# Kernel optimization log

Hardware: AMD Instinct MI355X
Metric: run time of the kernel (lower is better)

## Reference

```python
import jax, jax.numpy as jnp
import numpy as np
import math

B, S, D, H, M = 2, 2048, 1024, 16, 64
HD = D // H  # head_dim = 64


def setup_inputs() -> dict:
    key = jax.random.key(0)
    ks = jax.random.split(key, 16)
    inp = {
        "query": jax.random.normal(ks[0], (B, S, D), jnp.float32),
        "key": jax.random.normal(ks[1], (B, S, D), jnp.float32),
        "value": jax.random.normal(ks[2], (B, S, D), jnp.float32),
        "mask": jax.random.randint(ks[3], (B, 1, 1, S), 0, 2, jnp.int32),
        "Wq": jax.random.normal(ks[4], (D, D), jnp.float32) * 0.02,
        "bq": jnp.zeros((D,), jnp.float32),
        "Wk": jax.random.normal(ks[5], (D, D), jnp.float32) * 0.02,
        "bk": jnp.zeros((D,), jnp.float32),
        "Wv": jax.random.normal(ks[6], (D, D), jnp.float32) * 0.02,
        "bv": jnp.zeros((D,), jnp.float32),
        "Wo": jax.random.normal(ks[7], (D, D), jnp.float32) * 0.02,
        "bo": jnp.zeros((D,), jnp.float32),
        "m_k": jax.random.normal(ks[8], (1, M, D), jnp.float32) * (1.0 / HD),
        "m_v": jax.random.normal(ks[9], (1, M, D), jnp.float32) * (1.0 / M),
    }
    return inp


def reference(query, key, value, mask, Wq, bq, Wk, bk, Wv, bv, Wo, bo, m_k, m_v):
    b, nq, d = query.shape
    nk = key.shape[1]
    h, hd, m = H, HD, M
    scale = math.sqrt(hd)

    Q = query @ Wq.T + bq                      # [b, nq, d]
    K = key @ Wk.T + bk                        # [b, nk, d]
    V = value @ Wv.T + bv                      # [b, nk, d]

    mk = scale * jnp.broadcast_to(m_k, (b, m, d))           # sqrt(head_dim)*m_k
    mv = math.sqrt(m) * jnp.broadcast_to(m_v, (b, m, d))    # sqrt(m)*m_v

    K = jnp.concatenate([K, mk], axis=1)       # [b, nk+m, d]
    V = jnp.concatenate([V, mv], axis=1)

    Qh = Q.reshape(b, nq, h, hd).transpose(0, 2, 1, 3)           # [b,h,nq,hd]
    Kh = K.reshape(b, nk + m, h, hd).transpose(0, 2, 1, 3)       # [b,h,nk+m,hd]
    Vh = V.reshape(b, nk + m, h, hd).transpose(0, 2, 1, 3)

    energy = jnp.einsum('bhqd,bhkd->bhqk', Qh, Kh) / scale       # [b,h,nq,nk+m]
    # mask only the first nk key columns; memory slots are never masked
    masked = jnp.where(mask == 0, jnp.float32(-1e20), energy[..., :nk])
    energy = jnp.concatenate([masked, energy[..., nk:]], axis=-1)

    attention = jax.nn.softmax(energy, axis=-1)
    x = jnp.einsum('bhqk,bhkd->bhqd', attention, Vh)             # [b,h,nq,hd]
    x = x.transpose(0, 2, 1, 3).reshape(b, nq, d)
    return x @ Wo.T + bo
```

## Files before the change

kernel.cpp:

```cpp
#include <hip/hip_runtime.h>
#include <hip/hip_bf16.h>
#include <stdint.h>

#define B_  2
#define S_  2048
#define D_  1024
#define H_  16
#define HD_ 64
#define M_  64
#define SKM (S_ + M_)
#define LOG2E 1.44269504088896340736f

typedef __attribute__((ext_vector_type(8))) short s16x8;
typedef __attribute__((ext_vector_type(4))) float f32x4;
typedef __attribute__((ext_vector_type(16))) float f32x16;

#define GLOAD16(gp, lp) __builtin_amdgcn_global_load_lds( \
    (const __attribute__((address_space(1))) void*)(gp),  \
    (__attribute__((address_space(3))) void*)(lp), 16, 0, 0)

#define WAITVM(N) do { asm volatile("s_waitcnt vmcnt(" #N ")" ::: "memory"); \
                       __builtin_amdgcn_sched_barrier(0); } while (0)
#define BARRIER() do { asm volatile("" ::: "memory"); \
                       __builtin_amdgcn_s_barrier(); \
                       asm volatile("" ::: "memory"); } while (0)

__device__ __forceinline__ unsigned short f2bf(float f) {
  union { float f; unsigned int u; } v; v.f = f;
  unsigned int r = v.u + 0x7fffu + ((v.u >> 16) & 1u);
  return (unsigned short)(r >> 16);
}

__device__ __forceinline__ unsigned pkbf(float lo, float hi) {
  union { __hip_bfloat162 b; unsigned u; } t;
  t.b = __float22bfloat162_rn(make_float2(lo, hi));
  return t.u;
}

__global__ void compact_mask(const int* __restrict__ mask,
                             int* __restrict__ idx, int* __restrict__ cnt) {
  const int b = blockIdx.x;
  __shared__ int base, wsum[4];
  if (threadIdx.x == 0) base = 0;
  const int lane = threadIdx.x & 63, w = threadIdx.x >> 6;
  __syncthreads();
  for (int c = 0; c < S_; c += 256) {
    int key = c + threadIdx.x;
    int mv = mask[b * S_ + key];
    unsigned long long bal = __ballot(mv != 0);
    int pre = __popcll(bal & ((1ull << lane) - 1ull));
    if (lane == 0) wsum[w] = __popcll(bal);
    __syncthreads();
    int woff = 0;
    for (int i = 0; i < w; i++) woff += wsum[i];
    int tot = wsum[0] + wsum[1] + wsum[2] + wsum[3];
    if (mv) idx[b * S_ + base + woff + pre] = key;
    __syncthreads();
    if (threadIdx.x == 0) base += tot;
    __syncthreads();
  }
  if (threadIdx.x == 0) cnt[b] = base;
}

__global__ void cvt_all(const float* __restrict__ q,
                        const float* __restrict__ w0, const float* __restrict__ w1,
                        const float* __restrict__ w2, const float* __restrict__ w3,
                        unsigned short* __restrict__ qf,
                        unsigned short* __restrict__ o0, unsigned short* __restrict__ o1,
                        unsigned short* __restrict__ o2, unsigned short* __restrict__ o3) {
  size_t i = ((size_t)blockIdx.x * 256 + threadIdx.x) * 4;
  const float* in; unsigned short* out; size_t off;
  const size_t NQs = (size_t)B_ * S_ * D_;
  if (i < NQs) { in = q; out = qf; off = i; }
  else {
    size_t j = i - NQs;
    int wsel = (int)(j >> 20);
    off = j & ((1u << 20) - 1);
    in  = (wsel == 0) ? w0 : (wsel == 1) ? w1 : (wsel == 2) ? w2 : w3;
    out = (wsel == 0) ? o0 : (wsel == 1) ? o1 : (wsel == 2) ? o2 : o3;
  }
  float4 v = *(const float4*)&in[off];
  ushort4 o;
  o.x = f2bf(v.x); o.y = f2bf(v.y); o.z = f2bf(v.z); o.w = f2bf(v.w);
  *(ushort4*)&out[off] = o;
}

__global__ void cvt_kv_gather(const float* __restrict__ key, const float* __restrict__ value,
                              unsigned short* __restrict__ kf, unsigned short* __restrict__ vf,
                              const int* __restrict__ idx, const int* __restrict__ cnt) {
  int b = blockIdx.y, j = blockIdx.x;
  if (j >= cnt[b]) return;
  const float* in = blockIdx.z ? value : key;
  unsigned short* out = blockIdx.z ? vf : kf;
  int src = idx[b * S_ + j];
  const float* ip = in + ((size_t)(b * S_) + src) * D_;
  unsigned short* op = out + ((size_t)(b * S_) + j) * D_;
  int t = threadIdx.x * 4;
  float4 v = *(const float4*)&ip[t];
  ushort4 o;
  o.x = f2bf(v.x); o.y = f2bf(v.y); o.z = f2bf(v.z); o.w = f2bf(v.w);
  *(ushort4*)&op[t] = o;
}

__global__ void fill_mem(const float* __restrict__ mk, const float* __restrict__ mv,
                         unsigned short* __restrict__ Kb, unsigned short* __restrict__ VtG,
                         const int* __restrict__ cnt) {
  int i = blockIdx.x * 256 + threadIdx.x;
  int row = i >> 10, col = i & 1023;
  int hI = col >> 6, dd = col & 63;
  unsigned short kv = f2bf(8.0f * mk[i]);
  unsigned short vv = f2bf(8.0f * mv[i]);
#pragma unroll
  for (int b = 0; b < B_; b++) {
    int c = cnt[b];
    Kb[((size_t)(b * SKM) + c + row) * D_ + col] = kv;
    VtG[((size_t)(b * H_ + hI) * HD_ + dd) * SKM + c + row] = vv;
  }
}

__device__ __forceinline__ void gemm_core4(
    const unsigned short* __restrict__ A,
    const unsigned short* __restrict__ Bw,
    unsigned short* As, unsigned short* Bs,
    int mBase, int nBase, int K,
    int w, int lane, int wr, int wc, int lr, int lk,
    f32x4 acc[4][4]) {
  const int srow = w * 32 + (lane >> 2);
  const int cd = lane & 3;
  const int NT = K / 32;

#define STAGE_(buf, k0)                                                          \
  {                                                                              \
    _Pragma("unroll")                                                            \
    for (int i = 0; i < 2; i++) {                                                \
      int r = srow + i * 16;                                                     \
      int ca = cd ^ ((r >> 1) & 3);           \
      GLOAD16(&A[(size_t)(mBase + r) * K + (k0) + ca * 8],                       \
              &As[(buf) * (128 * 32) + (w * 32 + i * 16) * 32]);                 \
      GLOAD16(&Bw[(size_t)(nBase + r) * K + (k0) + ca * 8],                      \
              &Bs[(buf) * (128 * 32) + (w * 32 + i * 16) * 32]);                 \
    }                                                                            \
  }

  STAGE_(0, 0);
  STAGE_(1, 32);
  STAGE_(2, 64);
  for (int t = 0; t < NT; ++t) {
    const int cur = t & 3;
    if (t + 3 < NT) {
      STAGE_((t + 3) & 3, (t + 3) * 32);
      WAITVM(12);
    } else if (t + 3 == NT) {
      WAITVM(8);
    } else if (t + 2 == NT) {
      WAITVM(4);
    } else {
      WAITVM(0);
    }
    BARRIER();
    s16x8 af[4], bf[4];
#pragma unroll
    for (int mi = 0; mi < 4; mi++) {
      int row = wr * 64 + mi * 16 + lr;
      af[mi] = *(const s16x8*)&As[cur * (128 * 32) + row * 32 + ((lk ^ ((row >> 1) & 3)) << 3)];
    }
#pragma unroll
    for (int ni = 0; ni < 4; ni++) {
      int row = wc * 64 + ni * 16 + lr;
      bf[ni] = *(const s16x8*)&Bs[cur * (128 * 32) + row * 32 + ((lk ^ ((row >> 1) & 3)) << 3)];
    }
#pragma unroll
    for (int mi = 0; mi < 4; mi++)
#pragma unroll
      for (int ni = 0; ni < 4; ni++)
        acc[mi][ni] = __builtin_amdgcn_mfma_f32_16x16x32_bf16(af[mi], bf[ni], acc[mi][ni], 0, 0, 0);
    BARRIER();
  }
#undef STAGE_
}

__global__ __launch_bounds__(256)
void gemm_qkv(const unsigned short* __restrict__ qf, const unsigned short* __restrict__ kf,
              const unsigned short* __restrict__ vf,
              const unsigned short* __restrict__ wq, const unsigned short* __restrict__ wk,
              const unsigned short* __restrict__ wv,
              const float* __restrict__ bq, const float* __restrict__ bk,
              const float* __restrict__ bv,
              unsigned short* __restrict__ Qb, unsigned short* __restrict__ Kb,
              unsigned short* __restrict__ Vt,
              const int* __restrict__ cnt) {
  __shared__ __align__(16) unsigned short As[4 * 128 * 32];
  __shared__ __align__(16) unsigned short Bs[4 * 128 * 32];
  const int z = blockIdx.x >> 8;
  const int local = blockIdx.x & 255;
  const int ws = (local & 7) * 32 + (local >> 3);
  const int nBase = (ws & 7) * 128, mBase = (ws >> 3) * 128;
  if (z) {
    int c = (mBase < S_) ? cnt[0] : cnt[1];
    int lo = (mBase < S_) ? mBase : (mBase - S_);
    if (lo >= c) return;
  }
  const unsigned short* A  = (z == 0) ? qf : (z == 1) ? kf : vf;
  const unsigned short* Bw = (z == 0) ? wq : (z == 1) ? wk : wv;
  const float* bias        = (z == 0) ? bq : (z == 1) ? bk : bv;

  const int tid = threadIdx.x, lane = tid & 63;
  const int w = tid >> 6, wr = w >> 1, wc = w & 1;
  const int lr = lane & 15, lk = lane >> 4;

  const f32x4 fz = {0.f, 0.f, 0.f, 0.f};
  f32x4 acc[4][4];
#pragma unroll
  for (int i = 0; i < 4; i++)
#pragma unroll
    for (int j = 0; j < 4; j++) acc[i][j] = fz;

  gemm_core4(A, Bw, As, Bs, mBase, nBase, D_, w, lane, wr, wc, lr, lk, acc);

  const float alpha = (z == 0) ? 0.125f * LOG2E : 1.0f;
#pragma unroll
  for (int mi = 0; mi < 4; mi++)
#pragma unroll
    for (int ni = 0; ni < 4; ni++)
#pragma unroll
      for (int r = 0; r < 4; r++) {
        int gr = mBase + wr * 64 + mi * 16 + lk * 4 + r;
        int gc = nBase + wc * 64 + ni * 16 + lr;
        float v = (acc[mi][ni][r] + bias[gc]) * alpha;
        if (z == 2) {
          int bb = gr / S_, s = gr - bb * S_;
          int hI = gc >> 6, dd = gc & 63;
          Vt[((size_t)(bb * H_ + hI) * HD_ + dd) * SKM + s] = f2bf(v);
        } else if (z == 1) {
          int orow = gr + (gr / S_) * M_;
          Kb[(size_t)orow * D_ + gc] = f2bf(v);
        } else {
          Qb[(size_t)gr * D_ + gc] = f2bf(v);
        }
      }
}

__global__ __launch_bounds__(256)
void gemm_o(const unsigned short* __restrict__ A, const unsigned short* __restrict__ Bw,
            const float* __restrict__ bias, float* __restrict__ Cout) {
  __shared__ __align__(16) unsigned short As[4 * 128 * 32];
  __shared__ __align__(16) unsigned short Bs[4 * 128 * 32];
  const int local = blockIdx.x & 255;
  const int ws = (local & 7) * 32 + (local >> 3);
  const int nBase = (ws & 7) * 128, mBase = (ws >> 3) * 128;
  const int tid = threadIdx.x, lane = tid & 63;
  const int w = tid >> 6, wr = w >> 1, wc = w & 1;
  const int lr = lane & 15, lk = lane >> 4;

  const f32x4 fz = {0.f, 0.f, 0.f, 0.f};
  f32x4 acc[4][4];
#pragma unroll
  for (int i = 0; i < 4; i++)
#pragma unroll
    for (int j = 0; j < 4; j++) acc[i][j] = fz;

  gemm_core4(A, Bw, As, Bs, mBase, nBase, D_, w, lane, wr, wc, lr, lk, acc);

#pragma unroll
  for (int mi = 0; mi < 4; mi++)
#pragma unroll
    for (int ni = 0; ni < 4; ni++)
#pragma unroll
      for (int r = 0; r < 4; r++) {
        int gr = mBase + wr * 64 + mi * 16 + lk * 4 + r;
        int gc = nBase + wc * 64 + ni * 16 + lr;
        Cout[(size_t)gr * D_ + gc] = acc[mi][ni][r] + bias[gc];
      }
}

__global__ __launch_bounds__(512)
void attn_kernel(const unsigned short* __restrict__ Qb,
                 const unsigned short* __restrict__ Kb,
                 const unsigned short* __restrict__ VtG,
                 const int* __restrict__ cnt,
                 unsigned short* __restrict__ Xb) {
  __shared__ __align__(16) unsigned short Ks[64 * 64];
  __shared__ __align__(16) unsigned short Vs[64 * 64];

  const int tid = threadIdx.x, lane = tid & 63, w = tid >> 6;
  const int l31 = lane & 31, hh = lane >> 5;
  const int qt = blockIdx.x, h = blockIdx.y, b = blockIdx.z;

  const int total = cnt[b] + M_;
  const int nt = (total + 63) >> 6;

  const int r0 = tid >> 3, c0 = tid & 7;
  const int ck = c0 ^ (r0 & 7);
  const unsigned short* Kg = Kb + (size_t)b * SKM * D_ + (size_t)h * HD_;
  const unsigned short* Vg = VtG + (size_t)(b * H_ + h) * HD_ * SKM;

  const unsigned short* qp = Qb + ((size_t)(b * S_) + qt * 256 + w * 32 + l31) * D_ + h * HD_;
  s16x8 qf[4];
#pragma unroll
  for (int ds = 0; ds < 4; ds++) qf[ds] = *(const s16x8*)&qp[ds * 16 + hh * 8];

  f32x16 accO[2];
#pragma unroll
  for (int dt = 0; dt < 2; dt++)
#pragma unroll
    for (int j = 0; j < 16; j++) accO[dt][j] = 0.f;
  float m_r = -1e20f, l_r = 0.f;

  uint4 kr0, vr0;
  auto LOAD = [&](int kt) {
    kr0 = *(const uint4*)&Kg[(size_t)(kt * 64 + r0) * D_ + c0 * 8];
    vr0 = *(const uint4*)&Vg[(size_t)r0 * SKM + kt * 64 + c0 * 8];
  };
  LOAD(0);

  for (int kt = 0; kt < nt; ++kt) {
    __syncthreads();
    *(uint4*)&Ks[r0 * 64 + ck * 8] = kr0;
    *(uint4*)&Vs[r0 * 64 + ck * 8] = vr0;
    __syncthreads();
    if (kt + 1 < nt) LOAD(kt + 1);

    f32x16 p0, p1;
#pragma unroll
    for (int j = 0; j < 16; j++) { p0[j] = 0.f; p1[j] = 0.f; }
#pragma unroll
    for (int ds = 0; ds < 4; ds++) {
      s16x8 ka0 = *(const s16x8*)&Ks[l31 * 64 + (((ds * 2 + hh) ^ (l31 & 7)) << 3)];
      s16x8 ka1 = *(const s16x8*)&Ks[(32 + l31) * 64 + (((ds * 2 + hh) ^ (l31 & 7)) << 3)];
      p0 = __builtin_amdgcn_mfma_f32_32x32x16_bf16(ka0, qf[ds], p0, 0, 0, 0);
      p1 = __builtin_amdgcn_mfma_f32_32x32x16_bf16(ka1, qf[ds], p1, 0, 0, 0);
    }

    if (kt == nt - 1) {
      int valid = total - kt * 64;
#pragma unroll
      for (int j = 0; j < 16; j++) {
        int kl = (j & 3) + 8 * (j >> 2) + 4 * hh;
        if (kl >= valid) p0[j] = -1e30f;
        if (kl + 32 >= valid) p1[j] = -1e30f;
      }
    }

    float vmax = fmaxf(p0[0], p1[0]);
#pragma unroll
    for (int j = 1; j < 16; j++) vmax = fmaxf(vmax, fmaxf(p0[j], p1[j]));
    vmax = fmaxf(vmax, __shfl_xor(vmax, 32));
    if (!__all(vmax - m_r <= 8.0f)) {
      float mnew = fmaxf(m_r, vmax);
      float fac = __builtin_amdgcn_exp2f(m_r - mnew);
      m_r = mnew;
      l_r *= fac;
#pragma unroll
      for (int dt = 0; dt < 2; dt++)
#pragma unroll
        for (int j = 0; j < 16; j++) accO[dt][j] *= fac;
    }
    float sum = 0.f;
#pragma unroll
    for (int j = 0; j < 16; j++) {
      p0[j] = __builtin_amdgcn_exp2f(p0[j] - m_r); sum += p0[j];
      p1[j] = __builtin_amdgcn_exp2f(p1[j] - m_r); sum += p1[j];
    }
    sum += __shfl_xor(sum, 32);
    l_r += sum;

    s16x8 pf_[4];
#pragma unroll
    for (int ks = 0; ks < 4; ks++) {
      const int base = (ks & 1) * 8;
#define ELT(t) ((ks >= 2) ? p1[base + (t)] : p0[base + (t)])
      unsigned w0 = pkbf(ELT(0), ELT(1));
      unsigned w1 = pkbf(ELT(2), ELT(3));
      unsigned w2 = pkbf(ELT(4), ELT(5));
      unsigned w3 = pkbf(ELT(6), ELT(7));
#undef ELT
      unsigned s0 = hh ? w0 : w2;
      unsigned s1 = hh ? w1 : w3;
      unsigned g0 = (unsigned)__shfl_xor((int)s0, 32);
      unsigned g1 = (unsigned)__shfl_xor((int)s1, 32);
      union { s16x8 v; unsigned u[4]; } pf;
      pf.u[0] = hh ? g0 : w0;
      pf.u[1] = hh ? g1 : w1;
      pf.u[2] = hh ? w2 : g0;
      pf.u[3] = hh ? w3 : g1;
      pf_[ks] = pf.v;
    }

#pragma unroll
    for (int dt = 0; dt < 2; dt++)
#pragma unroll
      for (int ks = 0; ks < 4; ks++) {
        s16x8 va = *(const s16x8*)&Vs[(dt * 32 + l31) * 64 + (((ks * 2 + hh) ^ (l31 & 7)) << 3)];
        accO[dt] = __builtin_amdgcn_mfma_f32_32x32x16_bf16(va, pf_[ks], accO[dt], 0, 0, 0);
      }
  }

  float invl = 1.0f / l_r;
  size_t orow = ((size_t)(b * S_) + qt * 256 + w * 32 + l31) * D_ + h * HD_;
#pragma unroll
  for (int dt = 0; dt < 2; dt++)
#pragma unroll
    for (int j = 0; j < 16; j++) {
      int d = dt * 32 + (j & 3) + 8 * (j >> 2) + 4 * hh;
      Xb[orow + d] = f2bf(accO[dt][j] * invl);
    }
}

extern "C" void kernel_launch(void* const* d_in, const int* in_sizes, int n_in,
                              void* d_out, int out_size, void* d_ws, size_t ws_size,
                              hipStream_t stream) {
  const float* query = (const float*)d_in[0];
  const float* key   = (const float*)d_in[1];
  const float* value = (const float*)d_in[2];
  const int*   mask  = (const int*)d_in[3];
  const float* Wq    = (const float*)d_in[4];
  const float* bq    = (const float*)d_in[5];
  const float* Wk    = (const float*)d_in[6];
  const float* bk    = (const float*)d_in[7];
  const float* Wv    = (const float*)d_in[8];
  const float* bv    = (const float*)d_in[9];
  const float* Wo    = (const float*)d_in[10];
  const float* bo    = (const float*)d_in[11];
  const float* m_k   = (const float*)d_in[12];
  const float* m_v   = (const float*)d_in[13];

  const int NQ = B_ * S_ * D_;
  const int NW = D_ * D_;
  const int NK = B_ * SKM * D_;

  unsigned short* ws = (unsigned short*)d_ws;
  unsigned short* qf = ws;
  unsigned short* kf = qf + NQ;
  unsigned short* vf = kf + NQ;
  unsigned short* wq = vf + NQ;
  unsigned short* wk = wq + NW;
  unsigned short* wv = wk + NW;
  unsigned short* wo = wv + NW;
  unsigned short* Qb = wo + NW;
  unsigned short* Kb = Qb + NQ;
  unsigned short* Vt = Kb + NK;
  unsigned short* Xb = Vt + NK;
  int* idx = (int*)(Xb + NQ);
  int* cnt = idx + B_ * S_;

  compact_mask<<<B_, 256, 0, stream>>>(mask, idx, cnt);
  cvt_kv_gather<<<dim3(S_, B_, 2), 256, 0, stream>>>(key, value, kf, vf, idx, cnt);
  cvt_all<<<(NQ + 4 * NW) / 1024, 256, 0, stream>>>(query, Wq, Wk, Wv, Wo,
                                                    qf, wq, wk, wv, wo);

  gemm_qkv<<<768, 256, 0, stream>>>(qf, kf, vf, wq, wk, wv, bq, bk, bv, Qb, Kb, Vt, cnt);
  fill_mem<<<(M_ * D_) / 256, 256, 0, stream>>>(m_k, m_v, Kb, Vt, cnt);

  attn_kernel<<<dim3(S_ / 256, H_, B_), 512, 0, stream>>>(Qb, Kb, Vt, cnt, Xb);

  gemm_o<<<256, 256, 0, stream>>>(Xb, wo, bo, (float*)d_out);
}
```

Before: 141.3 us.

## Shrink GEMM tiles to 64x128 with double-buffered pipeline for more blocks

Halves the M tile of the QKV and output projection GEMMs from 128 to 64 rows, doubling the grid to 1536 and 512 blocks. The four-stage cp.async-style pipeline becomes a two-stage double buffer, which cuts LDS use per block. The goal is better occupancy and fewer idle CUs on the 256-CU part, where 256 blocks left gemm_o underfilled. In exchange each block reuses loaded data less, so more global traffic is needed per FLOP, and the shallower prefetch can hide less memory latency.

```diff
diff --git a/kernel.cpp b/kernel.cpp
--- a/kernel.cpp
+++ b/kernel.cpp
@@ -118,51 +118,48 @@
   }
 }
 
-__device__ __forceinline__ void gemm_core4(
+__device__ __forceinline__ void gemm_core64(
     const unsigned short* __restrict__ A,
     const unsigned short* __restrict__ Bw,
     unsigned short* As, unsigned short* Bs,
     int mBase, int nBase, int K,
-    int w, int lane, int wr, int wc, int lr, int lk,
-    f32x4 acc[4][4]) {
-  const int srow = w * 32 + (lane >> 2);
-  const int cd = lane & 3;
+    int tid, f32x4 acc[2][4]) {
+  const int lane = tid & 63, w = tid >> 6;
+  const int wr = w >> 1, wc = w & 1;
+  const int lr = lane & 15, lk = lane >> 4;
+  const int srA = tid >> 2, cdA = tid & 3;
+  const int srB = w * 32 + (lane >> 2), cdB = lane & 3;
+  const int caA = cdA ^ ((srA >> 1) & 3);
   const int NT = K / 32;
 
 #define STAGE_(buf, k0)                                                          \
   {                                                                              \
+    GLOAD16(&A[(size_t)(mBase + srA) * K + (k0) + caA * 8],                      \
+            &As[(buf) * (64 * 32) + (w * 16) * 32]);                             \
     _Pragma("unroll")                                                            \
     for (int i = 0; i < 2; i++) {                                                \
-      int r = srow + i * 16;                                                     \
-      int ca = cd ^ ((r >> 1) & 3);           \
-      GLOAD16(&A[(size_t)(mBase + r) * K + (k0) + ca * 8],                       \
-              &As[(buf) * (128 * 32) + (w * 32 + i * 16) * 32]);                 \
+      int r = srB + i * 16;                                                      \
+      int ca = cdB ^ ((r >> 1) & 3);                                             \
       GLOAD16(&Bw[(size_t)(nBase + r) * K + (k0) + ca * 8],                      \
               &Bs[(buf) * (128 * 32) + (w * 32 + i * 16) * 32]);                 \
     }                                                                            \
   }
 
   STAGE_(0, 0);
-  STAGE_(1, 32);
-  STAGE_(2, 64);
+  int cur = 0;
   for (int t = 0; t < NT; ++t) {
-    const int cur = t & 3;
-    if (t + 3 < NT) {
-      STAGE_((t + 3) & 3, (t + 3) * 32);
-      WAITVM(12);
-    } else if (t + 3 == NT) {
-      WAITVM(8);
-    } else if (t + 2 == NT) {
-      WAITVM(4);
+    if (t + 1 < NT) {
+      STAGE_(cur ^ 1, (t + 1) * 32);
+      WAITVM(3);
     } else {
       WAITVM(0);
     }
     BARRIER();
-    s16x8 af[4], bf[4];
-#pragma unroll
-    for (int mi = 0; mi < 4; mi++) {
-      int row = wr * 64 + mi * 16 + lr;
-      af[mi] = *(const s16x8*)&As[cur * (128 * 32) + row * 32 + ((lk ^ ((row >> 1) & 3)) << 3)];
+    s16x8 af[2], bf[4];
+#pragma unroll
+    for (int mi = 0; mi < 2; mi++) {
+      int row = wr * 32 + mi * 16 + lr;
+      af[mi] = *(const s16x8*)&As[cur * (64 * 32) + row * 32 + ((lk ^ ((row >> 1) & 3)) << 3)];
     }
 #pragma unroll
     for (int ni = 0; ni < 4; ni++) {
@@ -170,11 +167,12 @@
       bf[ni] = *(const s16x8*)&Bs[cur * (128 * 32) + row * 32 + ((lk ^ ((row >> 1) & 3)) << 3)];
     }
 #pragma unroll
-    for (int mi = 0; mi < 4; mi++)
+    for (int mi = 0; mi < 2; mi++)
 #pragma unroll
       for (int ni = 0; ni < 4; ni++)
         acc[mi][ni] = __builtin_amdgcn_mfma_f32_16x16x32_bf16(af[mi], bf[ni], acc[mi][ni], 0, 0, 0);
     BARRIER();
+    cur ^= 1;
   }
 #undef STAGE_
 }
@@ -189,16 +187,15 @@
               unsigned short* __restrict__ Qb, unsigned short* __restrict__ Kb,
               unsigned short* __restrict__ Vt,
               const int* __restrict__ cnt) {
-  __shared__ __align__(16) unsigned short As[4 * 128 * 32];
-  __shared__ __align__(16) unsigned short Bs[4 * 128 * 32];
-  const int z = blockIdx.x >> 8;
-  const int local = blockIdx.x & 255;
-  const int ws = (local & 7) * 32 + (local >> 3);
-  const int nBase = (ws & 7) * 128, mBase = (ws >> 3) * 128;
+  __shared__ __align__(16) unsigned short As[2 * 64 * 32];
+  __shared__ __align__(16) unsigned short Bs[2 * 128 * 32];
+  const int z = blockIdx.x >> 9;
+  const int local = blockIdx.x & 511;
+  const int wsz = (local & 7) * 64 + (local >> 3);
+  const int nBase = (wsz & 7) * 128, mBase = (wsz >> 3) * 64;
+  const int bb = (mBase >= S_);
   if (z) {
-    int c = (mBase < S_) ? cnt[0] : cnt[1];
-    int lo = (mBase < S_) ? mBase : (mBase - S_);
-    if (lo >= c) return;
+    if (mBase - bb * S_ >= cnt[bb]) return;
   }
   const unsigned short* A  = (z == 0) ? qf : (z == 1) ? kf : vf;
   const unsigned short* Bw = (z == 0) ? wq : (z == 1) ? wk : wv;
@@ -209,30 +206,30 @@
   const int lr = lane & 15, lk = lane >> 4;
 
   const f32x4 fz = {0.f, 0.f, 0.f, 0.f};
-  f32x4 acc[4][4];
-#pragma unroll
-  for (int i = 0; i < 4; i++)
+  f32x4 acc[2][4];
+#pragma unroll
+  for (int i = 0; i < 2; i++)
 #pragma unroll
     for (int j = 0; j < 4; j++) acc[i][j] = fz;
 
-  gemm_core4(A, Bw, As, Bs, mBase, nBase, D_, w, lane, wr, wc, lr, lk, acc);
+  gemm_core64(A, Bw, As, Bs, mBase, nBase, D_, tid, acc);
 
   const float alpha = (z == 0) ? 0.125f * LOG2E : 1.0f;
 #pragma unroll
-  for (int mi = 0; mi < 4; mi++)
+  for (int mi = 0; mi < 2; mi++)
 #pragma unroll
     for (int ni = 0; ni < 4; ni++)
 #pragma unroll
       for (int r = 0; r < 4; r++) {
-        int gr = mBase + wr * 64 + mi * 16 + lk * 4 + r;
+        int gr = mBase + wr * 32 + mi * 16 + lk * 4 + r;
         int gc = nBase + wc * 64 + ni * 16 + lr;
         float v = (acc[mi][ni][r] + bias[gc]) * alpha;
         if (z == 2) {
-          int bb = gr / S_, s = gr - bb * S_;
+          int s = gr - bb * S_;
           int hI = gc >> 6, dd = gc & 63;
           Vt[((size_t)(bb * H_ + hI) * HD_ + dd) * SKM + s] = f2bf(v);
         } else if (z == 1) {
-          int orow = gr + (gr / S_) * M_;
+          int orow = gr + bb * M_;
           Kb[(size_t)orow * D_ + gc] = f2bf(v);
         } else {
           Qb[(size_t)gr * D_ + gc] = f2bf(v);
@@ -243,31 +240,31 @@
 __global__ __launch_bounds__(256)
 void gemm_o(const unsigned short* __restrict__ A, const unsigned short* __restrict__ Bw,
             const float* __restrict__ bias, float* __restrict__ Cout) {
-  __shared__ __align__(16) unsigned short As[4 * 128 * 32];
-  __shared__ __align__(16) unsigned short Bs[4 * 128 * 32];
-  const int local = blockIdx.x & 255;
-  const int ws = (local & 7) * 32 + (local >> 3);
-  const int nBase = (ws & 7) * 128, mBase = (ws >> 3) * 128;
+  __shared__ __align__(16) unsigned short As[2 * 64 * 32];
+  __shared__ __align__(16) unsigned short Bs[2 * 128 * 32];
+  const int local = blockIdx.x & 511;
+  const int wsz = (local & 7) * 64 + (local >> 3);
+  const int nBase = (wsz & 7) * 128, mBase = (wsz >> 3) * 64;
   const int tid = threadIdx.x, lane = tid & 63;
   const int w = tid >> 6, wr = w >> 1, wc = w & 1;
   const int lr = lane & 15, lk = lane >> 4;
 
   const f32x4 fz = {0.f, 0.f, 0.f, 0.f};
-  f32x4 acc[4][4];
-#pragma unroll
-  for (int i = 0; i < 4; i++)
+  f32x4 acc[2][4];
+#pragma unroll
+  for (int i = 0; i < 2; i++)
 #pragma unroll
     for (int j = 0; j < 4; j++) acc[i][j] = fz;
 
-  gemm_core4(A, Bw, As, Bs, mBase, nBase, D_, w, lane, wr, wc, lr, lk, acc);
-
-#pragma unroll
-  for (int mi = 0; mi < 4; mi++)
+  gemm_core64(A, Bw, As, Bs, mBase, nBase, D_, tid, acc);
+
+#pragma unroll
+  for (int mi = 0; mi < 2; mi++)
 #pragma unroll
     for (int ni = 0; ni < 4; ni++)
 #pragma unroll
       for (int r = 0; r < 4; r++) {
-        int gr = mBase + wr * 64 + mi * 16 + lk * 4 + r;
+        int gr = mBase + wr * 32 + mi * 16 + lk * 4 + r;
         int gc = nBase + wc * 64 + ni * 16 + lr;
         Cout[(size_t)gr * D_ + gc] = acc[mi][ni][r] + bias[gc];
       }
@@ -448,10 +445,10 @@
   cvt_all<<<(NQ + 4 * NW) / 1024, 256, 0, stream>>>(query, Wq, Wk, Wv, Wo,
                                                     qf, wq, wk, wv, wo);
 
-  gemm_qkv<<<768, 256, 0, stream>>>(qf, kf, vf, wq, wk, wv, bq, bk, bv, Qb, Kb, Vt, cnt);
+  gemm_qkv<<<1536, 256, 0, stream>>>(qf, kf, vf, wq, wk, wv, bq, bk, bv, Qb, Kb, Vt, cnt);
   fill_mem<<<(M_ * D_) / 256, 256, 0, stream>>>(m_k, m_v, Kb, Vt, cnt);
 
   attn_kernel<<<dim3(S_ / 256, H_, B_), 512, 0, stream>>>(Qb, Kb, Vt, cnt, Xb);
 
-  gemm_o<<<256, 256, 0, stream>>>(Xb, wo, bo, (float*)d_out);
-}
+  gemm_o<<<512, 256, 0, stream>>>(Xb, wo, bo, (float*)d_out);
+}
```

Result: no change. 142.5 us (+0.9%).
